# Performance work log

Hardware: AMD Instinct MI355X
Metric: run time of the kernel (lower is better)

Reference implementation:

```python
import jax, jax.numpy as jnp
import numpy as np

N, E, H = 50000, 800000, 64  # nodes, edges, hidden
EPS = 1e-5
SLOPE = 0.2  # LeakyReLU negative slope


def setup_inputs() -> dict:
    key = jax.random.key(0)
    ks = jax.random.split(key, 8)
    return {
        "x": jax.random.normal(ks[0], (N, H), dtype=jnp.float32),
        "edge_weight": jax.random.uniform(ks[1], (E,), dtype=jnp.float32),
        "edge_index": jax.random.randint(ks[2], (2, E), 0, N, dtype=jnp.int64),
        # Linear weights, torch convention [out_features, in_features], bias=False
        "w1": jax.random.normal(ks[3], (H, 2 * H), dtype=jnp.float32) * 0.05,
        "w2": jax.random.normal(ks[4], (H, H), dtype=jnp.float32) * 0.05,
        "w3": jax.random.normal(ks[5], (H, H), dtype=jnp.float32) * 0.05,
        # LayerNorm affine params
        "g1": jnp.ones((2 * H,), jnp.float32), "b1": jnp.zeros((2 * H,), jnp.float32),
        "g2": jnp.ones((H,), jnp.float32), "b2": jnp.zeros((H,), jnp.float32),
        "g3": jnp.ones((H,), jnp.float32), "b3": jnp.zeros((H,), jnp.float32),
    }


def _ln_act_lin(h, g, b, w):
    # LayerNorm -> LeakyReLU(0.2) -> Linear(bias=False), as in MLP(norm='layer')
    mu = jnp.mean(h, axis=-1, keepdims=True)
    var = jnp.mean((h - mu) ** 2, axis=-1, keepdims=True)
    h = (h - mu) * jax.lax.rsqrt(var + EPS) * g + b
    h = jnp.where(h > 0, h, SLOPE * h)
    return h @ w.T


def reference(x, edge_weight, edge_index, w1, w2, w3, g1, b1, g2, b2, g3, b3):
    src, tgt = edge_index[0], edge_index[1]  # x_j = source, x_i = target
    x_j = x[src]                              # [E, H] gather
    x_i = x[tgt]                              # [E, H] gather
    m = jnp.concatenate([x_i, edge_weight[:, None] * (x_j - x_i)], axis=-1)  # [E, 2H]
    m = _ln_act_lin(m, g1, b1, w1)
    m = _ln_act_lin(m, g2, b2, w2)
    m = _ln_act_lin(m, g3, b3, w3)            # [E, H]
    agg = jax.ops.segment_max(m, tgt, num_segments=N)  # EdgeConv aggr='max'
    agg = jnp.where(jnp.isfinite(agg), agg, 0.0)       # isolated nodes -> 0
    return agg + x                             # residual (ResBlock)
```

## Files before the change

kernel.cpp:

```cpp
#include <hip/hip_runtime.h>

#define NN 50000
#define NE 800000

#define CNT_OFF   0u
#define BASE_OFF  (1u << 18)
#define SLOT_OFF  (1u << 19)
#define M_OFF     (1u << 22)
#define WS_NEEDED ((size_t)(1u << 22) + (size_t)NE * 64u * 2u)

typedef __bf16 bf16x8 __attribute__((ext_vector_type(8)));
typedef float f32x16 __attribute__((ext_vector_type(16)));

union U4 { unsigned u[4]; __bf16 h[8]; bf16x8 v; };

__device__ __forceinline__ unsigned pkpair(float a, float b) {
  union { unsigned u; __bf16 h[2]; } r;
  r.h[0] = (__bf16)a; r.h[1] = (__bf16)b;
  return r.u;
}
__device__ __forceinline__ float bflo(unsigned u) { return __uint_as_float(u << 16); }
__device__ __forceinline__ float bfhi(unsigned u) { return __uint_as_float(u & 0xFFFF0000u); }

extern "C" __global__ void __launch_bounds__(256)
scatter_kernel(const int* __restrict__ ei, unsigned* __restrict__ cnt,
               unsigned* __restrict__ slot) {
  const int e = blockIdx.x * 256 + threadIdx.x;
  if (e < NE) {
    int t = ei[NE + e];
    t = min(max(t, 0), NN - 1);
    slot[e] = atomicAdd(cnt + t, 1u);
  }
}

extern "C" __global__ void __launch_bounds__(1024)
scan_kernel(const unsigned* __restrict__ cnt, unsigned* __restrict__ base) {
  __shared__ unsigned wsum[16];
  __shared__ unsigned carry;
  const int tid = threadIdx.x;
  const int wv = tid >> 6, ln = tid & 63;
  if (tid == 0) carry = 0;
  __syncthreads();
  for (int off = 0; off < NN; off += 1024) {
    const int i = off + tid;
    const unsigned v = (i < NN) ? cnt[i] : 0u;
    unsigned s = v;
    #pragma unroll
    for (int d = 1; d < 64; d <<= 1) {
      const unsigned t = __shfl_up(s, d);
      if (ln >= d) s += t;
    }
    if (ln == 63) wsum[wv] = s;
    __syncthreads();
    if (tid == 0) {
      unsigned run = carry;
      #pragma unroll
      for (int k = 0; k < 16; ++k) { const unsigned t = wsum[k]; wsum[k] = run; run += t; }
      carry = run;
    }
    __syncthreads();
    if (i < NN) base[i] = wsum[wv] + s - v;
    __syncthreads();
  }
  if (tid == 0) base[NN] = carry;
}

extern "C" __global__ void __launch_bounds__(256)
edge_mlp_kernel(const float* __restrict__ x, const float* __restrict__ ew,
                const int* __restrict__ ei, const float* __restrict__ w1,
                const float* __restrict__ w2, const float* __restrict__ w3,
                const float* __restrict__ g1, const float* __restrict__ b1,
                const float* __restrict__ g2, const float* __restrict__ b2,
                const float* __restrict__ g3, const float* __restrict__ b3,
                const unsigned* __restrict__ basep, const unsigned* __restrict__ slot,
                unsigned* __restrict__ agg ,
                unsigned short* __restrict__ mbuf ) {
  __shared__ unsigned lds_w[8192];
  const int tid = threadIdx.x;

  #pragma unroll 1
  for (int s = tid; s < 1024; s += 256) {
    const int F = s >> 6, L = s & 63;
    const int t = F >> 1, mt = F & 1;
    const int gg = L >> 5, o = (L & 31) + 32 * mt;
    const float* p = w1 + o * 128 + 16 * t + 8 * gg;
    unsigned* d = &lds_w[(unsigned)(F * 64 + L) * 4u];
    d[0] = pkpair(p[0], p[1]); d[1] = pkpair(p[2], p[3]);
    d[2] = pkpair(p[4], p[5]); d[3] = pkpair(p[6], p[7]);
  }
  #pragma unroll 1
  for (int s = tid; s < 1024; s += 256) {
    const int which = s >> 9, r = s & 511;
    const int F = r >> 6, L = r & 63;
    const int t = F >> 1, mt = F & 1;
    const int gg = L >> 5, o = (L & 31) + 32 * mt;
    const float* W = which ? w3 : w2;
    const float* p = W + o * 64 + 16 * t + 4 * gg;
    unsigned* d = &lds_w[(unsigned)((16 + which * 8 + F) * 64 + L) * 4u];
    d[0] = pkpair(p[0], p[1]); d[1] = pkpair(p[2], p[3]);
    d[2] = pkpair(p[8], p[9]); d[3] = pkpair(p[10], p[11]);
  }
  __syncthreads();

  const int lane = tid & 63;
  const int el = lane & 31;
  const int g = lane >> 5;
  const bf16x8* wfrag = (const bf16x8*)lds_w;

  const int wid = blockIdx.x * 4 + (tid >> 6);
  const int nw = gridDim.x * 4;

  for (int tile = wid; tile < (NE / 32); tile += nw) {
    const float* g1p = g1; const float* b1p = b1;
    const float* g2p = g2; const float* b2p = b2;
    const float* g3p = g3; const float* b3p = b3;
    asm volatile("" : "+s"(g1p), "+s"(b1p), "+s"(g2p), "+s"(b2p), "+s"(g3p), "+s"(b3p));

    const int e = tile * 32 + el;
    int vsrc = ei[e];
    int vtgt = ei[NE + e];
    vsrc = min(max(vsrc, 0), NN - 1);
    vtgt = min(max(vtgt, 0), NN - 1);
    const float wgt = ew[e];

    const float* xi = x + (size_t)vtgt * 64 + 8 * g;
    const float* xj = x + (size_t)vsrc * 64 + 8 * g;

    unsigned mp[32];
    float sum = 0.f, ssq = 0.f;
    #pragma unroll
    for (int t = 0; t < 4; ++t) {
      float4 a = *(const float4*)(xi + 16 * t);
      float4 b = *(const float4*)(xi + 16 * t + 4);
      float4 c = *(const float4*)(xj + 16 * t);
      float4 d4 = *(const float4*)(xj + 16 * t + 4);
      float lo[8] = {a.x, a.y, a.z, a.w, b.x, b.y, b.z, b.w};
      float up[8] = {wgt * (c.x - a.x), wgt * (c.y - a.y), wgt * (c.z - a.z), wgt * (c.w - a.w),
                     wgt * (d4.x - b.x), wgt * (d4.y - b.y), wgt * (d4.z - b.z), wgt * (d4.w - b.w)};
      #pragma unroll
      for (int p = 0; p < 4; ++p) {
        mp[4 * t + p] = pkpair(lo[2 * p], lo[2 * p + 1]);
        mp[16 + 4 * t + p] = pkpair(up[2 * p], up[2 * p + 1]);
      }
      #pragma unroll
      for (int j = 0; j < 8; ++j) {
        sum += lo[j] + up[j];
        ssq += lo[j] * lo[j] + up[j] * up[j];
      }
    }

    sum += __shfl_xor(sum, 32);
    ssq += __shfl_xor(ssq, 32);
    const float mean1 = sum * (1.f / 128.f);
    const float rstd1 = rsqrtf(ssq * (1.f / 128.f) - mean1 * mean1 + 1e-5f);
    const float c01 = -mean1 * rstd1;

    U4 B1[8];
    #pragma unroll
    for (int t = 0; t < 8; ++t) {
      const int kb = ((t < 4) ? 16 * t : 64 + 16 * (t - 4)) + 8 * g;
      float4 ga = *(const float4*)(g1p + kb);
      float4 gb = *(const float4*)(g1p + kb + 4);
      float4 ba = *(const float4*)(b1p + kb);
      float4 bb = *(const float4*)(b1p + kb + 4);
      float gv[8] = {ga.x, ga.y, ga.z, ga.w, gb.x, gb.y, gb.z, gb.w};
      float bv[8] = {ba.x, ba.y, ba.z, ba.w, bb.x, bb.y, bb.z, bb.w};
      #pragma unroll
      for (int p = 0; p < 4; ++p) {
        const unsigned u = mp[4 * t + p];
        float v0 = fmaf(bflo(u), rstd1, c01);
        float v1 = fmaf(bfhi(u), rstd1, c01);
        v0 = fmaf(v0, gv[2 * p], bv[2 * p]);
        v1 = fmaf(v1, gv[2 * p + 1], bv[2 * p + 1]);
        v0 = v0 > 0.f ? v0 : 0.2f * v0;
        v1 = v1 > 0.f ? v1 : 0.2f * v1;
        B1[t].h[2 * p] = (__bf16)v0;
        B1[t].h[2 * p + 1] = (__bf16)v1;
      }
    }

    f32x16 C0, C1;
    #pragma unroll
    for (int i = 0; i < 16; ++i) { C0[i] = 0.f; C1[i] = 0.f; }
    #pragma unroll
    for (int t = 0; t < 8; ++t) {
      C0 = __builtin_amdgcn_mfma_f32_32x32x16_bf16(wfrag[(2 * t + 0) * 64 + lane], B1[t].v, C0, 0, 0, 0);
      C1 = __builtin_amdgcn_mfma_f32_32x32x16_bf16(wfrag[(2 * t + 1) * 64 + lane], B1[t].v, C1, 0, 0, 0);
    }

    float s2 = 0.f, q2 = 0.f;
    #pragma unroll
    for (int i = 0; i < 16; ++i) {
      s2 += C0[i] + C1[i];
      q2 += C0[i] * C0[i] + C1[i] * C1[i];
    }
    s2 += __shfl_xor(s2, 32); q2 += __shfl_xor(q2, 32);
    const float mean2 = s2 * (1.f / 64.f);
    const float rstd2 = rsqrtf(q2 * (1.f / 64.f) - mean2 * mean2 + 1e-5f);
    const float c02 = -mean2 * rstd2;

    U4 B2[4];
    #pragma unroll
    for (int t2 = 0; t2 < 4; ++t2) {
      const int kb = 16 * t2 + 4 * g;
      float4 gA = *(const float4*)(g2p + kb);
      float4 gB = *(const float4*)(g2p + kb + 8);
      float4 bA = *(const float4*)(b2p + kb);
      float4 bB = *(const float4*)(b2p + kb + 8);
      float gv[8] = {gA.x, gA.y, gA.z, gA.w, gB.x, gB.y, gB.z, gB.w};
      float bv[8] = {bA.x, bA.y, bA.z, bA.w, bB.x, bB.y, bB.z, bB.w};
      #pragma unroll
      for (int j = 0; j < 8; ++j) {
        const int reg = 4 * (2 * (t2 & 1) + (j >> 2)) + (j & 3);
        float v = (t2 >> 1) ? C1[reg] : C0[reg];
        v = fmaf(v, rstd2, c02);
        v = fmaf(v, gv[j], bv[j]);
        v = v > 0.f ? v : 0.2f * v;
        B2[t2].h[j] = (__bf16)v;
      }
    }

    f32x16 D0, D1;
    #pragma unroll
    for (int i = 0; i < 16; ++i) { D0[i] = 0.f; D1[i] = 0.f; }
    #pragma unroll
    for (int t2 = 0; t2 < 4; ++t2) {
      D0 = __builtin_amdgcn_mfma_f32_32x32x16_bf16(wfrag[(16 + 2 * t2 + 0) * 64 + lane], B2[t2].v, D0, 0, 0, 0);
      D1 = __builtin_amdgcn_mfma_f32_32x32x16_bf16(wfrag[(16 + 2 * t2 + 1) * 64 + lane], B2[t2].v, D1, 0, 0, 0);
    }

    float s3 = 0.f, q3 = 0.f;
    #pragma unroll
    for (int i = 0; i < 16; ++i) {
      s3 += D0[i] + D1[i];
      q3 += D0[i] * D0[i] + D1[i] * D1[i];
    }
    s3 += __shfl_xor(s3, 32); q3 += __shfl_xor(q3, 32);
    const float mean3 = s3 * (1.f / 64.f);
    const float rstd3 = rsqrtf(q3 * (1.f / 64.f) - mean3 * mean3 + 1e-5f);
    const float c03 = -mean3 * rstd3;

    U4 B3[4];
    #pragma unroll
    for (int t2 = 0; t2 < 4; ++t2) {
      const int kb = 16 * t2 + 4 * g;
      float4 gA = *(const float4*)(g3p + kb);
      float4 gB = *(const float4*)(g3p + kb + 8);
      float4 bA = *(const float4*)(b3p + kb);
      float4 bB = *(const float4*)(b3p + kb + 8);
      float gv[8] = {gA.x, gA.y, gA.z, gA.w, gB.x, gB.y, gB.z, gB.w};
      float bv[8] = {bA.x, bA.y, bA.z, bA.w, bB.x, bB.y, bB.z, bB.w};
      #pragma unroll
      for (int j = 0; j < 8; ++j) {
        const int reg = 4 * (2 * (t2 & 1) + (j >> 2)) + (j & 3);
        float v = (t2 >> 1) ? D1[reg] : D0[reg];
        v = fmaf(v, rstd3, c03);
        v = fmaf(v, gv[j], bv[j]);
        v = v > 0.f ? v : 0.2f * v;
        B3[t2].h[j] = (__bf16)v;
      }
    }

    f32x16 F0, F1;
    #pragma unroll
    for (int i = 0; i < 16; ++i) { F0[i] = 0.f; F1[i] = 0.f; }
    #pragma unroll
    for (int t2 = 0; t2 < 4; ++t2) {
      F0 = __builtin_amdgcn_mfma_f32_32x32x16_bf16(wfrag[(24 + 2 * t2 + 0) * 64 + lane], B3[t2].v, F0, 0, 0, 0);
      F1 = __builtin_amdgcn_mfma_f32_32x32x16_bf16(wfrag[(24 + 2 * t2 + 1) * 64 + lane], B3[t2].v, F1, 0, 0, 0);
    }

    if (mbuf) {
      const unsigned pos = basep[vtgt] + slot[e];
      unsigned short* row = mbuf + (size_t)pos * 64;
      #pragma unroll
      for (int mt = 0; mt < 2; ++mt) {
        #pragma unroll
        for (int q = 0; q < 4; ++q) {
          const int f0 = 8 * q + 4 * g + 32 * mt;
          uint2 pk;
          pk.x = mt ? pkpair(F1[4 * q + 0], F1[4 * q + 1]) : pkpair(F0[4 * q + 0], F0[4 * q + 1]);
          pk.y = mt ? pkpair(F1[4 * q + 2], F1[4 * q + 3]) : pkpair(F0[4 * q + 2], F0[4 * q + 3]);
          *(uint2*)(row + f0) = pk;
        }
      }
    } else {
      unsigned* ap = agg + (size_t)vtgt * 64;
      #pragma unroll
      for (int mt = 0; mt < 2; ++mt) {
        #pragma unroll
        for (int reg = 0; reg < 16; ++reg) {
          const int f = (reg & 3) + 8 * (reg >> 2) + 4 * g + 32 * mt;
          float v = mt ? F1[reg] : F0[reg];
          unsigned u = __float_as_uint(v);
          unsigned key = (u & 0x80000000u) ? ~u : (u | 0x80000000u);
          atomicMax(ap + f, key);
        }
      }
    }
  }
}

extern "C" __global__ void __launch_bounds__(256)
gather_max_kernel(const float* __restrict__ x, const unsigned short* __restrict__ mbuf,
                  const unsigned* __restrict__ base, float* __restrict__ out) {
  const int node = blockIdx.x * 4 + (threadIdx.x >> 6);
  const int lane = threadIdx.x & 63;
  if (node >= NN) return;

  const unsigned b0 = base[node];
  const unsigned deg = base[node + 1] - b0;

  const unsigned short* p = mbuf + (size_t)b0 * 64 + lane * 4;
  const int krow = lane >> 4;
  float4 acc = {-INFINITY, -INFINITY, -INFINITY, -INFINITY};
  const int nch = ((int)deg + 3) >> 2;
  for (int c = 0; c < nch; ++c) {
    if (c * 4 + krow < (int)deg) {
      const ushort4 v = *(const ushort4*)(p + (size_t)c * 256);
      acc.x = fmaxf(acc.x, __uint_as_float((unsigned)v.x << 16));
      acc.y = fmaxf(acc.y, __uint_as_float((unsigned)v.y << 16));
      acc.z = fmaxf(acc.z, __uint_as_float((unsigned)v.z << 16));
      acc.w = fmaxf(acc.w, __uint_as_float((unsigned)v.w << 16));
    }
  }
  #pragma unroll
  for (int d = 16; d < 64; d <<= 1) {
    acc.x = fmaxf(acc.x, __shfl_xor(acc.x, d));
    acc.y = fmaxf(acc.y, __shfl_xor(acc.y, d));
    acc.z = fmaxf(acc.z, __shfl_xor(acc.z, d));
    acc.w = fmaxf(acc.w, __shfl_xor(acc.w, d));
  }
  if (lane < 16) {
    const size_t o = (size_t)node * 64 + lane * 4;
    const float4 xr = *(const float4*)(x + o);
    float4 r;
    r.x = (acc.x >= -3.0e38f ? acc.x : 0.f) + xr.x;
    r.y = (acc.y >= -3.0e38f ? acc.y : 0.f) + xr.y;
    r.z = (acc.z >= -3.0e38f ? acc.z : 0.f) + xr.z;
    r.w = (acc.w >= -3.0e38f ? acc.w : 0.f) + xr.w;
    *(float4*)(out + o) = r;
  }
}

extern "C" __global__ void __launch_bounds__(256)
finalize_kernel(const float* __restrict__ x, unsigned* __restrict__ out) {
  const int i = blockIdx.x * 256 + threadIdx.x;
  if (i < NN * 64) {
    const unsigned key = out[i];
    const unsigned u = (key & 0x80000000u) ? (key & 0x7FFFFFFFu) : ~key;
    float v = __uint_as_float(u);
    if (((u >> 23) & 0xFFu) == 0xFFu) v = 0.f;
    ((float*)out)[i] = v + x[i];
  }
}

extern "C" void kernel_launch(void* const* d_in, const int* in_sizes, int n_in,
                              void* d_out, int out_size, void* d_ws, size_t ws_size,
                              hipStream_t stream) {
  (void)in_sizes; (void)n_in; (void)out_size;
  const float* x  = (const float*)d_in[0];
  const float* ew = (const float*)d_in[1];
  const int*   ei = (const int*)d_in[2];
  const float* w1 = (const float*)d_in[3];
  const float* w2 = (const float*)d_in[4];
  const float* w3 = (const float*)d_in[5];
  const float* g1 = (const float*)d_in[6];
  const float* b1 = (const float*)d_in[7];
  const float* g2 = (const float*)d_in[8];
  const float* b2 = (const float*)d_in[9];
  const float* g3 = (const float*)d_in[10];
  const float* b3 = (const float*)d_in[11];

  if (ws_size >= WS_NEEDED) {
    unsigned* cnt  = (unsigned*)((char*)d_ws + CNT_OFF);
    unsigned* base = (unsigned*)((char*)d_ws + BASE_OFF);
    unsigned* slot = (unsigned*)((char*)d_ws + SLOT_OFF);
    unsigned short* mbuf = (unsigned short*)((char*)d_ws + M_OFF);

    hipMemsetAsync(cnt, 0, (size_t)NN * sizeof(unsigned), stream);
    scatter_kernel<<<(NE + 255) / 256, 256, 0, stream>>>(ei, cnt, slot);
    scan_kernel<<<1, 1024, 0, stream>>>(cnt, base);
    edge_mlp_kernel<<<1024, 256, 0, stream>>>(x, ew, ei, w1, w2, w3,
                                              g1, b1, g2, b2, g3, b3,
                                              base, slot, nullptr, mbuf);
    gather_max_kernel<<<(NN + 3) / 4, 256, 0, stream>>>(x, mbuf, base, (float*)d_out);
  } else {
    unsigned* agg = (unsigned*)d_out;
    hipMemsetAsync(d_out, 0, (size_t)NN * 64 * sizeof(float), stream);
    edge_mlp_kernel<<<1024, 256, 0, stream>>>(x, ew, ei, w1, w2, w3,
                                              g1, b1, g2, b2, g3, b3,
                                              nullptr, nullptr, agg, nullptr);
    finalize_kernel<<<(NN * 64 + 255) / 256, 256, 0, stream>>>(x, (unsigned*)d_out);
  }
}
```

Measured before the change: 342.9 us.

## Process edges in target-sorted order via CSR edge-id list with prefetch

Replaces the slot-based scatter with a full counting sort: count, a multi-block three-phase scan, and a fill kernel that writes edge ids into CSR order. The edge MLP then walks edges in sorted order, so x[tgt] gathers gain locality and mbuf rows are written contiguously without the basep/slot lookups. It also software-prefetches the next tile's edge indices and weights, and doubles the grid to 2048 blocks. The cost is extra kernel launches and an indirect eid load per edge.

```diff
diff --git a/kernel.cpp b/kernel.cpp
--- a/kernel.cpp
+++ b/kernel.cpp
@@ -2,12 +2,16 @@
 
 #define NN 50000
 #define NE 800000
+#define NT (NE / 32)
 
 #define CNT_OFF   0u
-#define BASE_OFF  (1u << 18)
-#define SLOT_OFF  (1u << 19)
+#define CNT2_OFF  200704u
+#define BASE_OFF  401408u
+#define PART_OFF  601856u
+#define EID_OFF   606208u
 #define M_OFF     (1u << 22)
 #define WS_NEEDED ((size_t)(1u << 22) + (size_t)NE * 64u * 2u)
+#define PB 196
 
 typedef __bf16 bf16x8 __attribute__((ext_vector_type(8)));
 typedef float f32x16 __attribute__((ext_vector_type(16)));
@@ -23,46 +27,73 @@
 __device__ __forceinline__ float bfhi(unsigned u) { return __uint_as_float(u & 0xFFFF0000u); }
 
 extern "C" __global__ void __launch_bounds__(256)
-scatter_kernel(const int* __restrict__ ei, unsigned* __restrict__ cnt,
-               unsigned* __restrict__ slot) {
+count_kernel(const int* __restrict__ ei, unsigned* __restrict__ cnt) {
   const int e = blockIdx.x * 256 + threadIdx.x;
   if (e < NE) {
     int t = ei[NE + e];
     t = min(max(t, 0), NN - 1);
-    slot[e] = atomicAdd(cnt + t, 1u);
-  }
-}
-
-extern "C" __global__ void __launch_bounds__(1024)
-scan_kernel(const unsigned* __restrict__ cnt, unsigned* __restrict__ base) {
-  __shared__ unsigned wsum[16];
-  __shared__ unsigned carry;
-  const int tid = threadIdx.x;
-  const int wv = tid >> 6, ln = tid & 63;
-  if (tid == 0) carry = 0;
+    atomicAdd(cnt + t, 1u);
+  }
+}
+
+extern "C" __global__ void __launch_bounds__(256)
+scan_a_kernel(const unsigned* __restrict__ cnt, unsigned* __restrict__ partial) {
+  __shared__ unsigned wsum[4];
+  const int t = threadIdx.x, wv = t >> 6, ln = t & 63;
+  const int i = blockIdx.x * 256 + t;
+  unsigned v = (i < NN) ? cnt[i] : 0u;
+  #pragma unroll
+  for (int d = 1; d < 64; d <<= 1) v += (unsigned)__shfl_up((int)v, d) * (ln >= d ? 1u : 0u);
+  if (ln == 63) wsum[wv] = v;
   __syncthreads();
-  for (int off = 0; off < NN; off += 1024) {
-    const int i = off + tid;
-    const unsigned v = (i < NN) ? cnt[i] : 0u;
-    unsigned s = v;
-    #pragma unroll
-    for (int d = 1; d < 64; d <<= 1) {
-      const unsigned t = __shfl_up(s, d);
-      if (ln >= d) s += t;
-    }
-    if (ln == 63) wsum[wv] = s;
-    __syncthreads();
-    if (tid == 0) {
-      unsigned run = carry;
-      #pragma unroll
-      for (int k = 0; k < 16; ++k) { const unsigned t = wsum[k]; wsum[k] = run; run += t; }
-      carry = run;
-    }
-    __syncthreads();
-    if (i < NN) base[i] = wsum[wv] + s - v;
-    __syncthreads();
-  }
-  if (tid == 0) base[NN] = carry;
+  if (t == 0) partial[blockIdx.x] = wsum[0] + wsum[1] + wsum[2] + wsum[3];
+}
+
+extern "C" __global__ void __launch_bounds__(256)
+scan_b_kernel(unsigned* __restrict__ partial, unsigned* __restrict__ base) {
+  __shared__ unsigned wsum[4];
+  const int t = threadIdx.x, wv = t >> 6, ln = t & 63;
+  const unsigned v = (t < PB) ? partial[t] : 0u;
+  unsigned s = v;
+  #pragma unroll
+  for (int d = 1; d < 64; d <<= 1) s += (unsigned)__shfl_up((int)s, d) * (ln >= d ? 1u : 0u);
+  if (ln == 63) wsum[wv] = s;
+  __syncthreads();
+  unsigned woff = 0;
+  #pragma unroll
+  for (int k = 0; k < 4; ++k) woff += (k < wv) ? wsum[k] : 0u;
+  if (t < PB) partial[t] = woff + s - v;
+  if (t == 255) base[NN] = woff + s;
+}
+
+extern "C" __global__ void __launch_bounds__(256)
+scan_c_kernel(const unsigned* __restrict__ cnt, const unsigned* __restrict__ partial,
+              unsigned* __restrict__ base) {
+  __shared__ unsigned wsum[4];
+  const int t = threadIdx.x, wv = t >> 6, ln = t & 63;
+  const int i = blockIdx.x * 256 + t;
+  const unsigned v = (i < NN) ? cnt[i] : 0u;
+  unsigned s = v;
+  #pragma unroll
+  for (int d = 1; d < 64; d <<= 1) s += (unsigned)__shfl_up((int)s, d) * (ln >= d ? 1u : 0u);
+  if (ln == 63) wsum[wv] = s;
+  __syncthreads();
+  unsigned woff = 0;
+  #pragma unroll
+  for (int k = 0; k < 4; ++k) woff += (k < wv) ? wsum[k] : 0u;
+  if (i < NN) base[i] = partial[blockIdx.x] + woff + s - v;
+}
+
+extern "C" __global__ void __launch_bounds__(256)
+fill_kernel(const int* __restrict__ ei, const unsigned* __restrict__ base,
+            unsigned* __restrict__ cnt2, unsigned* __restrict__ eid) {
+  const int e = blockIdx.x * 256 + threadIdx.x;
+  if (e < NE) {
+    int t = ei[NE + e];
+    t = min(max(t, 0), NN - 1);
+    const unsigned pos = base[t] + atomicAdd(cnt2 + t, 1u);
+    eid[pos] = (unsigned)e;
+  }
 }
 
 extern "C" __global__ void __launch_bounds__(256)
@@ -72,7 +103,7 @@
                 const float* __restrict__ g1, const float* __restrict__ b1,
                 const float* __restrict__ g2, const float* __restrict__ b2,
                 const float* __restrict__ g3, const float* __restrict__ b3,
-                const unsigned* __restrict__ basep, const unsigned* __restrict__ slot,
+                const unsigned* __restrict__ eid ,
                 unsigned* __restrict__ agg ,
                 unsigned short* __restrict__ mbuf ) {
   __shared__ unsigned lds_w[8192];
@@ -110,18 +141,25 @@
   const int wid = blockIdx.x * 4 + (tid >> 6);
   const int nw = gridDim.x * 4;
 
-  for (int tile = wid; tile < (NE / 32); tile += nw) {
+  int tile = wid;
+  int pe = 0, pvs = 0, pvt = 0; float pw = 0.f;
+  if (tile < NT) {
+    const int p0 = tile * 32 + el;
+    pe = eid ? (int)eid[p0] : p0;
+    pvs = min(max(ei[pe], 0), NN - 1);
+    pvt = min(max(ei[NE + pe], 0), NN - 1);
+    pw = ew[pe];
+  }
+
+  while (tile < NT) {
     const float* g1p = g1; const float* b1p = b1;
     const float* g2p = g2; const float* b2p = b2;
     const float* g3p = g3; const float* b3p = b3;
     asm volatile("" : "+s"(g1p), "+s"(b1p), "+s"(g2p), "+s"(b2p), "+s"(g3p), "+s"(b3p));
 
-    const int e = tile * 32 + el;
-    int vsrc = ei[e];
-    int vtgt = ei[NE + e];
-    vsrc = min(max(vsrc, 0), NN - 1);
-    vtgt = min(max(vtgt, 0), NN - 1);
-    const float wgt = ew[e];
+    const int p = tile * 32 + el;
+    const int e = pe, vsrc = pvs, vtgt = pvt;
+    const float wgt = pw;
 
     const float* xi = x + (size_t)vtgt * 64 + 8 * g;
     const float* xj = x + (size_t)vsrc * 64 + 8 * g;
@@ -138,15 +176,24 @@
       float up[8] = {wgt * (c.x - a.x), wgt * (c.y - a.y), wgt * (c.z - a.z), wgt * (c.w - a.w),
                      wgt * (d4.x - b.x), wgt * (d4.y - b.y), wgt * (d4.z - b.z), wgt * (d4.w - b.w)};
       #pragma unroll
-      for (int p = 0; p < 4; ++p) {
-        mp[4 * t + p] = pkpair(lo[2 * p], lo[2 * p + 1]);
-        mp[16 + 4 * t + p] = pkpair(up[2 * p], up[2 * p + 1]);
+      for (int pp = 0; pp < 4; ++pp) {
+        mp[4 * t + pp] = pkpair(lo[2 * pp], lo[2 * pp + 1]);
+        mp[16 + 4 * t + pp] = pkpair(up[2 * pp], up[2 * pp + 1]);
       }
       #pragma unroll
       for (int j = 0; j < 8; ++j) {
         sum += lo[j] + up[j];
         ssq += lo[j] * lo[j] + up[j] * up[j];
       }
+    }
+
+    const int ntile = tile + nw;
+    if (ntile < NT) {
+      const int pn = ntile * 32 + el;
+      pe = eid ? (int)eid[pn] : pn;
+      pvs = min(max(ei[pe], 0), NN - 1);
+      pvt = min(max(ei[NE + pe], 0), NN - 1);
+      pw = ew[pe];
     }
 
     sum += __shfl_xor(sum, 32);
@@ -166,16 +213,16 @@
       float gv[8] = {ga.x, ga.y, ga.z, ga.w, gb.x, gb.y, gb.z, gb.w};
       float bv[8] = {ba.x, ba.y, ba.z, ba.w, bb.x, bb.y, bb.z, bb.w};
       #pragma unroll
-      for (int p = 0; p < 4; ++p) {
-        const unsigned u = mp[4 * t + p];
+      for (int pp = 0; pp < 4; ++pp) {
+        const unsigned u = mp[4 * t + pp];
         float v0 = fmaf(bflo(u), rstd1, c01);
         float v1 = fmaf(bfhi(u), rstd1, c01);
-        v0 = fmaf(v0, gv[2 * p], bv[2 * p]);
-        v1 = fmaf(v1, gv[2 * p + 1], bv[2 * p + 1]);
+        v0 = fmaf(v0, gv[2 * pp], bv[2 * pp]);
+        v1 = fmaf(v1, gv[2 * pp + 1], bv[2 * pp + 1]);
         v0 = v0 > 0.f ? v0 : 0.2f * v0;
         v1 = v1 > 0.f ? v1 : 0.2f * v1;
-        B1[t].h[2 * p] = (__bf16)v0;
-        B1[t].h[2 * p + 1] = (__bf16)v1;
+        B1[t].h[2 * pp] = (__bf16)v0;
+        B1[t].h[2 * pp + 1] = (__bf16)v1;
       }
     }
 
@@ -271,8 +318,7 @@
     }
 
     if (mbuf) {
-      const unsigned pos = basep[vtgt] + slot[e];
-      unsigned short* row = mbuf + (size_t)pos * 64;
+      unsigned short* row = mbuf + (size_t)p * 64;
       #pragma unroll
       for (int mt = 0; mt < 2; ++mt) {
         #pragma unroll
@@ -298,6 +344,8 @@
         }
       }
     }
+
+    tile = ntile;
   }
 }
 
@@ -373,24 +421,29 @@
   const float* b3 = (const float*)d_in[11];
 
   if (ws_size >= WS_NEEDED) {
-    unsigned* cnt  = (unsigned*)((char*)d_ws + CNT_OFF);
-    unsigned* base = (unsigned*)((char*)d_ws + BASE_OFF);
-    unsigned* slot = (unsigned*)((char*)d_ws + SLOT_OFF);
+    unsigned* cnt   = (unsigned*)((char*)d_ws + CNT_OFF);
+    unsigned* cnt2  = (unsigned*)((char*)d_ws + CNT2_OFF);
+    unsigned* base  = (unsigned*)((char*)d_ws + BASE_OFF);
+    unsigned* part  = (unsigned*)((char*)d_ws + PART_OFF);
+    unsigned* eid   = (unsigned*)((char*)d_ws + EID_OFF);
     unsigned short* mbuf = (unsigned short*)((char*)d_ws + M_OFF);
 
-    hipMemsetAsync(cnt, 0, (size_t)NN * sizeof(unsigned), stream);
-    scatter_kernel<<<(NE + 255) / 256, 256, 0, stream>>>(ei, cnt, slot);
-    scan_kernel<<<1, 1024, 0, stream>>>(cnt, base);
-    edge_mlp_kernel<<<1024, 256, 0, stream>>>(x, ew, ei, w1, w2, w3,
+    hipMemsetAsync(d_ws, 0, BASE_OFF, stream);
+    count_kernel<<<(NE + 255) / 256, 256, 0, stream>>>(ei, cnt);
+    scan_a_kernel<<<PB, 256, 0, stream>>>(cnt, part);
+    scan_b_kernel<<<1, 256, 0, stream>>>(part, base);
+    scan_c_kernel<<<PB, 256, 0, stream>>>(cnt, part, base);
+    fill_kernel<<<(NE + 255) / 256, 256, 0, stream>>>(ei, base, cnt2, eid);
+    edge_mlp_kernel<<<2048, 256, 0, stream>>>(x, ew, ei, w1, w2, w3,
                                               g1, b1, g2, b2, g3, b3,
-                                              base, slot, nullptr, mbuf);
+                                              eid, nullptr, mbuf);
     gather_max_kernel<<<(NN + 3) / 4, 256, 0, stream>>>(x, mbuf, base, (float*)d_out);
   } else {
     unsigned* agg = (unsigned*)d_out;
     hipMemsetAsync(d_out, 0, (size_t)NN * 64 * sizeof(float), stream);
     edge_mlp_kernel<<<1024, 256, 0, stream>>>(x, ew, ei, w1, w2, w3,
                                               g1, b1, g2, b2, g3, b3,
-                                              nullptr, nullptr, agg, nullptr);
+                                              nullptr, agg, nullptr);
     finalize_kernel<<<(NN * 64 + 255) / 256, 256, 0, stream>>>(x, (unsigned*)d_out);
   }
 }
```

Result: no change. 342.7 us (-0.1%).
